# Kernel optimization log

Hardware: AMD Instinct MI355X
Metric: run time of the kernel (lower is better)

The kernel has to match this reference:

```python
import jax, jax.numpy as jnp
import numpy as np

N_NODES = 10000
N_EDGES = 320000
IN_FEATS = 256
NUM_HEADS = 8
OUT_FEATS = 64
NEG_SLOPE = 0.2


def setup_inputs() -> dict:
    key = jax.random.key(0)
    k = jax.random.split(key, 7)
    feat = jax.random.normal(k[0], (N_NODES, IN_FEATS), dtype=jnp.float32)
    W = jax.random.normal(k[1], (IN_FEATS, NUM_HEADS * OUT_FEATS), dtype=jnp.float32) * (1.0 / np.sqrt(IN_FEATS))
    attn_l = jax.random.normal(k[2], (1, NUM_HEADS, OUT_FEATS), dtype=jnp.float32) * 0.1
    attn_r = jax.random.normal(k[3], (1, NUM_HEADS, OUT_FEATS), dtype=jnp.float32) * 0.1
    adj = jax.random.uniform(k[4], (N_NODES, N_NODES), dtype=jnp.float32)
    src = jax.random.randint(k[5], (N_EDGES,), 0, N_NODES, dtype=jnp.int32)
    dst = jax.random.randint(k[6], (N_EDGES,), 0, N_NODES, dtype=jnp.int32)
    return {"feat": feat, "W": W, "attn_l": attn_l, "attn_r": attn_r,
            "adj": adj, "src": src, "dst": dst, "idx": 0}


def reference(feat, W, attn_l, attn_r, adj, src, dst, idx):
    N = feat.shape[0]
    # node projection: [N, H, D]
    ft = (feat @ W).reshape(N, NUM_HEADS, OUT_FEATS)
    # per-node attention logits [N, H]
    el = jnp.sum(ft * attn_l, axis=-1)
    er = jnp.sum(ft * attn_r, axis=-1)
    # u_add_v on edges + LeakyReLU -> [E, H]
    e = el[src] + er[dst]
    e = jnp.where(e > 0, e, NEG_SLOPE * e)
    # edge softmax: segment softmax over destination node
    m = jax.ops.segment_max(e, dst, num_segments=N)          # [N, H]
    ex = jnp.exp(e - m[dst])                                  # [E, H]
    s = jax.ops.segment_sum(ex, dst, num_segments=N)          # [N, H]
    a = ex / s[dst]                                           # [E, H]
    # vectorized adjacency masking (replaces per-edge Python loop)
    a = a * adj[src + idx, dst + idx][:, None]                # [E, H]
    # u_mul_e + scatter-sum aggregation -> [N, H, D]
    msg = ft[src] * a[:, :, None]                             # [E, H, D]
    rst = jax.ops.segment_sum(msg, dst, num_segments=N)
    return rst
```

## Files before the change

kernel.cpp:

```cpp
#include <hip/hip_runtime.h>
#include <hip/hip_bf16.h>
#include <cstdint>
#include <cstddef>

#define IN_FEATS 256
#define NUM_HEADS 8
#define HD 512
#define CH 64
#define ELLCAP 128

typedef __attribute__((ext_vector_type(8))) short bf16x8;
typedef __attribute__((ext_vector_type(4))) float f32x4;

__device__ inline unsigned short bf16_bits(float f) {
    unsigned x = __float_as_uint(f);
    x += 0x7fffu + ((x >> 16) & 1u);
    return (unsigned short)(x >> 16);
}


__global__ __launch_bounds__(256) void k0_kernel(const float* __restrict__ W,
                                                 const float* __restrict__ feat,
                                                 int* __restrict__ deg,
                                                 unsigned short* __restrict__ Wt,
                                                 unsigned short* __restrict__ featb,
                                                 int M) {
    const int b = blockIdx.x;
    const int t = threadIdx.x;
    if (b < 40) {
        int i = b * 256 + t;
        if (i < M) deg[i] = 0;
        return;
    }
    if (b < 72) {
        __shared__ float tile[64][65];
        const int bb = b - 40;
        const int h = bb >> 2;
        const int k0 = (bb & 3) * 64;
#pragma unroll 4
        for (int it = 0; it < 16; ++it) {
            int r = it * 4 + (t >> 6);
            int c = t & 63;
            tile[r][c] = W[(size_t)(k0 + r) * HD + h * 64 + c];
        }
        __syncthreads();
#pragma unroll 4
        for (int it = 0; it < 16; ++it) {
            int c = it * 4 + (t >> 6);
            int k = t & 63;
            Wt[((size_t)h * 64 + c) * IN_FEATS + k0 + k] = bf16_bits(tile[k][c]);
        }
        return;
    }
    {
        size_t base = (size_t)(b - 72) * 1024 + (size_t)t * 4;
        if (base < (size_t)M * IN_FEATS) {
            float4 v = *(const float4*)(feat + base);
            ushort4 o;
            o.x = bf16_bits(v.x);
            o.y = bf16_bits(v.y);
            o.z = bf16_bits(v.z);
            o.w = bf16_bits(v.w);
            *(ushort4*)(featb + base) = o;
        }
    }
}


__global__ __launch_bounds__(256) void k1_kernel(const int* __restrict__ src,
                                                 const int* __restrict__ dst,
                                                 int* __restrict__ deg,
                                                 int* __restrict__ ell,
                                                 const unsigned short* __restrict__ featb,
                                                 const float* __restrict__ al,
                                                 const float* __restrict__ ar,
                                                 const unsigned short* __restrict__ Wt,
                                                 float* __restrict__ el,
                                                 float* __restrict__ er,
                                                 signed char* __restrict__ ftq,
                                                 float* __restrict__ scaleb,
                                                 int E, int M, int nb_ft) {
    const int b = blockIdx.x;
    const int t = threadIdx.x;
    if (b >= nb_ft) {
        int i = (b - nb_ft) * 256 + t;
        if (i < E) {
            int d = dst[i];
            int r = atomicAdd(&deg[d], 1);
            if (r < ELLCAP) ell[(size_t)d * ELLCAP + r] = src[i];
        }
        return;
    }
    {
        const int id = b;
        const int NBX = (M + 63) / 64;
        const int bx = id % NBX;
        const int by = id / NBX;
        const int lane = t & 63, wv = t >> 6;
        const int n0 = bx * 64 + wv * 16;
        const int r = lane & 15;
        const int kg = lane >> 4;
        const int arow = min(n0 + r, M - 1);
        const short* aptr = (const short*)featb + (size_t)arow * IN_FEATS + kg * 8;
        const short* bptr = (const short*)Wt + ((size_t)by * 64 + r) * IN_FEATS + kg * 8;
        f32x4 acc[4];
#pragma unroll
        for (int c = 0; c < 4; ++c) acc[c] = (f32x4){0.f, 0.f, 0.f, 0.f};
#pragma unroll
        for (int kk = 0; kk < 128; kk += 32) {
            bf16x8 a0 = *(const bf16x8*)(aptr + kk);
            bf16x8 a1 = *(const bf16x8*)(aptr + 128 + kk);
#pragma unroll
            for (int c = 0; c < 4; ++c) {
                bf16x8 b0 = *(const bf16x8*)(bptr + (size_t)c * 16 * IN_FEATS + kk);
                bf16x8 b1 = *(const bf16x8*)(bptr + (size_t)c * 16 * IN_FEATS + 128 + kk);
                acc[c] = __builtin_amdgcn_mfma_f32_16x16x32_bf16(a0, b0, acc[c], 0, 0, 0);
                acc[c] = __builtin_amdgcn_mfma_f32_16x16x32_bf16(a1, b1, acc[c], 0, 0, 0);
            }
        }
        float alv[4], arv[4];
#pragma unroll
        for (int c = 0; c < 4; ++c) {
            alv[c] = al[by * 64 + c * 16 + r];
            arv[c] = ar[by * 64 + c * 16 + r];
        }
        float iscale[4], sc[4], pl[4], pr[4];
#pragma unroll
        for (int i = 0; i < 4; ++i) {
            float m = fmaxf(fmaxf(fabsf(acc[0][i]), fabsf(acc[1][i])),
                            fmaxf(fabsf(acc[2][i]), fabsf(acc[3][i])));
            float l = acc[0][i] * alv[0] + acc[1][i] * alv[1] +
                      acc[2][i] * alv[2] + acc[3][i] * alv[3];
            float q = acc[0][i] * arv[0] + acc[1][i] * arv[1] +
                      acc[2][i] * arv[2] + acc[3][i] * arv[3];
#pragma unroll
            for (int off = 1; off < 16; off <<= 1) {
                m = fmaxf(m, __shfl_xor(m, off));
                l += __shfl_xor(l, off);
                q += __shfl_xor(q, off);
            }
            sc[i] = m * (1.0f / 127.0f);
            iscale[i] = (m > 1e-30f) ? (127.0f / m) : 0.f;
            pl[i] = l;
            pr[i] = q;
        }
        const int orow0 = n0 + kg * 4;
        if (r == 0) {
#pragma unroll
            for (int i = 0; i < 4; ++i) {
                int rr = orow0 + i;
                if (rr < M) {
                    scaleb[rr * NUM_HEADS + by] = sc[i];
                    el[rr * NUM_HEADS + by] = pl[i];
                    er[rr * NUM_HEADS + by] = pr[i];
                }
            }
        }
#pragma unroll
        for (int c = 0; c < 4; ++c) {
#pragma unroll
            for (int i = 0; i < 4; ++i) {
                int rr = orow0 + i;
                if (rr < M) {
                    int q = __float2int_rn(acc[c][i] * iscale[i]);
                    q = max(-127, min(127, q));
                    ftq[(size_t)rr * HD + by * 64 + c * 16 + r] = (signed char)q;
                }
            }
        }
    }
}


__global__ __launch_bounds__(256) void agg_kernel(
    const signed char* __restrict__ ftq, const float* __restrict__ scaleb,
    const float* __restrict__ el, const float* __restrict__ er,
    const float* __restrict__ adj, const int* __restrict__ deg,
    const int* __restrict__ ell, const int* __restrict__ idxp,
    float* __restrict__ out, int M) {
    const int n = blockIdx.x;
    const int t = threadIdx.x;
    const int h = t >> 5;
    const int cnt = min(deg[n], ELLCAP);
    if (cnt == 0) {
        *(float2*)(out + (size_t)n * HD + 2 * t) = make_float2(0.f, 0.f);
        return;
    }
    const int lane = t & 63, wv = t >> 6;
    const int j0 = t >> 2;
    const int hg = t & 3;
    const int idx = idxp[0];
    const float* adj_col = adj + (size_t)idx * M + (n + idx);
    const int* erow = ell + (size_t)n * ELLCAP;

    __shared__ float w_lds[2][CH][8];
    __shared__ int s_lds[2][CH];
    __shared__ float partial[4][4][2];
    __shared__ float inv_s[8];

    const float2 er2 = *(const float2*)&er[n * NUM_HEADS + 2 * hg];

    float2 ssum = make_float2(0.f, 0.f);
    float2 acc = make_float2(0.f, 0.f);
    int s_r = 0;
    float2 w_r = make_float2(0.f, 0.f);
    auto stage = [&](int base) {
        int j = base + j0;
        if (j < cnt) {
            s_r = erow[j];
            float2 e2 = *(const float2*)&el[s_r * NUM_HEADS + 2 * hg];
            float2 sc2 = *(const float2*)&scaleb[s_r * NUM_HEADS + 2 * hg];
            float av = adj_col[(size_t)s_r * M];
            float ex = e2.x + er2.x; ex = (ex > 0.f) ? ex : 0.2f * ex;
            float ey = e2.y + er2.y; ey = (ey > 0.f) ? ey : 0.2f * ey;
            float px = __expf(ex), py = __expf(ey);
            ssum.x += px; ssum.y += py;
            w_r = make_float2(px * av * sc2.x, py * av * sc2.y);
        }
    };
    auto write_lds = [&](int buf, int base) {
        int j = base + j0;
        if (j < cnt) {
            *(float2*)&w_lds[buf][j0][2 * hg] = w_r;
            if (hg == 0) s_lds[buf][j0] = s_r;
        }
    };
    int buf = 0;
    stage(0);
    write_lds(0, 0);
    __syncthreads();
    for (int base = 0; base < cnt; base += CH) {
        const bool more = (base + CH) < cnt;
        if (more) stage(base + CH);
        int c = min(CH, cnt - base);
        const int* srow = &s_lds[buf][0];
        const float* wrow = &w_lds[buf][0][0];
#pragma unroll 4
        for (int jj = 0; jj < c; ++jj) {
            int s = srow[jj];
            unsigned short v = *(const unsigned short*)(ftq + (size_t)s * HD + 2 * t);
            float fx = (float)(signed char)(v & 0xff);
            float fy = (float)(signed char)(v >> 8);
            float w = wrow[jj * 8 + h];
            acc.x = fmaf(w, fx, acc.x);
            acc.y = fmaf(w, fy, acc.y);
        }
        if (more) {
            write_lds(buf ^ 1, base + CH);
            __syncthreads();
            buf ^= 1;
        }
    }
    float sx = ssum.x, sy = ssum.y;
#pragma unroll
    for (int off = 4; off < 64; off <<= 1) {
        sx += __shfl_xor(sx, off);
        sy += __shfl_xor(sy, off);
    }
    if (lane < 4) {
        partial[wv][hg][0] = sx;
        partial[wv][hg][1] = sy;
    }
    __syncthreads();
    if (t < 8) {
        int hgg = t >> 1, comp = t & 1;
        inv_s[t] = 1.f / (partial[0][hgg][comp] + partial[1][hgg][comp] +
                          partial[2][hgg][comp] + partial[3][hgg][comp]);
    }
    __syncthreads();
    const float inv = inv_s[h];
    *(float2*)(out + (size_t)n * HD + 2 * t) = make_float2(acc.x * inv, acc.y * inv);
}


extern "C" void kernel_launch(void* const* d_in, const int* in_sizes, int n_in,
                              void* d_out, int out_size, void* d_ws, size_t ws_size,
                              hipStream_t stream) {
    const float* feat   = (const float*)d_in[0];
    const float* W      = (const float*)d_in[1];
    const float* attn_l = (const float*)d_in[2];
    const float* attn_r = (const float*)d_in[3];
    const float* adj    = (const float*)d_in[4];
    const int*   src    = (const int*)d_in[5];
    const int*   dst    = (const int*)d_in[6];
    const int*   idxp   = (const int*)d_in[7];
    float* out = (float*)d_out;

    const int M = in_sizes[0] / IN_FEATS;
    const int E = in_sizes[5];

    char* ws = (char*)d_ws;
    size_t off = 0;
    auto alloc = [&](size_t bytes) -> void* {
        off = (off + 255) & ~(size_t)255;
        void* p = ws + off;
        off += bytes;
        return p;
    };
    signed char* ftq      = (signed char*)alloc((size_t)M * HD);
    unsigned short* featb = (unsigned short*)alloc((size_t)M * IN_FEATS * sizeof(short));
    float* scaleb         = (float*)alloc((size_t)M * NUM_HEADS * sizeof(float));
    unsigned short* Wt    = (unsigned short*)alloc((size_t)HD * IN_FEATS * sizeof(short));
    float* el        = (float*)alloc((size_t)M * NUM_HEADS * sizeof(float));
    float* er        = (float*)alloc((size_t)M * NUM_HEADS * sizeof(float));
    int*   deg       = (int*)alloc((size_t)M * sizeof(int));
    int*   ell       = (int*)alloc((size_t)M * ELLCAP * sizeof(int));

    const int nb_cv = ((int)((size_t)M * IN_FEATS / 1024));
    k0_kernel<<<72 + nb_cv, 256, 0, stream>>>(W, feat, deg, Wt, featb, M);

    const int nb_sc = (E + 255) / 256;
    const int NBX = (M + 63) / 64;
    const int nb_ft = NBX * NUM_HEADS;
    k1_kernel<<<nb_ft + nb_sc, 256, 0, stream>>>(src, dst, deg, ell,
                                                 featb, attn_l, attn_r, Wt, el, er,
                                                 ftq, scaleb, E, M, nb_ft);

    agg_kernel<<<M, 256, 0, stream>>>(ftq, scaleb, el, er, adj, deg, ell, idxp, out, M);
}
```

Baseline: 89.79 us.

## Fuse feat bf16 conversion into GEMM and compute four heads per block

The separate fp32-to-bf16 conversion pass over feat and its workspace buffer are removed. The projection kernel now loads fp32 feat directly, converts it to bf16 in registers, and keeps the A fragments resident while each block computes four heads instead of one. This cuts a full write and read of the bf16 copy, and it reads feat twice rather than eight times. In exchange, GEMM blocks drop to a quarter as many and each uses far more accumulator registers (64 floats plus 8 A fragments), which may lower occupancy.

```diff
diff --git a/kernel.cpp b/kernel.cpp
--- a/kernel.cpp
+++ b/kernel.cpp
@@ -20,10 +20,8 @@
 
 
 __global__ __launch_bounds__(256) void k0_kernel(const float* __restrict__ W,
-                                                 const float* __restrict__ feat,
                                                  int* __restrict__ deg,
                                                  unsigned short* __restrict__ Wt,
-                                                 unsigned short* __restrict__ featb,
                                                  int M) {
     const int b = blockIdx.x;
     const int t = threadIdx.x;
@@ -32,37 +30,22 @@
         if (i < M) deg[i] = 0;
         return;
     }
-    if (b < 72) {
-        __shared__ float tile[64][65];
-        const int bb = b - 40;
-        const int h = bb >> 2;
-        const int k0 = (bb & 3) * 64;
+    __shared__ float tile[64][65];
+    const int bb = b - 40;
+    const int h = bb >> 2;
+    const int k0 = (bb & 3) * 64;
 #pragma unroll 4
-        for (int it = 0; it < 16; ++it) {
-            int r = it * 4 + (t >> 6);
-            int c = t & 63;
-            tile[r][c] = W[(size_t)(k0 + r) * HD + h * 64 + c];
-        }
-        __syncthreads();
+    for (int it = 0; it < 16; ++it) {
+        int r = it * 4 + (t >> 6);
+        int c = t & 63;
+        tile[r][c] = W[(size_t)(k0 + r) * HD + h * 64 + c];
+    }
+    __syncthreads();
 #pragma unroll 4
-        for (int it = 0; it < 16; ++it) {
-            int c = it * 4 + (t >> 6);
-            int k = t & 63;
-            Wt[((size_t)h * 64 + c) * IN_FEATS + k0 + k] = bf16_bits(tile[k][c]);
-        }
-        return;
-    }
-    {
-        size_t base = (size_t)(b - 72) * 1024 + (size_t)t * 4;
-        if (base < (size_t)M * IN_FEATS) {
-            float4 v = *(const float4*)(feat + base);
-            ushort4 o;
-            o.x = bf16_bits(v.x);
-            o.y = bf16_bits(v.y);
-            o.z = bf16_bits(v.z);
-            o.w = bf16_bits(v.w);
-            *(ushort4*)(featb + base) = o;
-        }
+    for (int it = 0; it < 16; ++it) {
+        int c = it * 4 + (t >> 6);
+        int k = t & 63;
+        Wt[((size_t)h * 64 + c) * IN_FEATS + k0 + k] = bf16_bits(tile[k][c]);
     }
 }
 
@@ -71,7 +54,7 @@
                                                  const int* __restrict__ dst,
                                                  int* __restrict__ deg,
                                                  int* __restrict__ ell,
-                                                 const unsigned short* __restrict__ featb,
+                                                 const float* __restrict__ feat,
                                                  const float* __restrict__ al,
                                                  const float* __restrict__ ar,
                                                  const unsigned short* __restrict__ Wt,
@@ -92,79 +75,98 @@
         return;
     }
     {
-        const int id = b;
         const int NBX = (M + 63) / 64;
-        const int bx = id % NBX;
-        const int by = id / NBX;
+        const int bx = b % NBX;
+        const int hg2 = b / NBX;
         const int lane = t & 63, wv = t >> 6;
         const int n0 = bx * 64 + wv * 16;
         const int r = lane & 15;
         const int kg = lane >> 4;
         const int arow = min(n0 + r, M - 1);
-        const short* aptr = (const short*)featb + (size_t)arow * IN_FEATS + kg * 8;
-        const short* bptr = (const short*)Wt + ((size_t)by * 64 + r) * IN_FEATS + kg * 8;
-        f32x4 acc[4];
-#pragma unroll
-        for (int c = 0; c < 4; ++c) acc[c] = (f32x4){0.f, 0.f, 0.f, 0.f};
-#pragma unroll
-        for (int kk = 0; kk < 128; kk += 32) {
-            bf16x8 a0 = *(const bf16x8*)(aptr + kk);
-            bf16x8 a1 = *(const bf16x8*)(aptr + 128 + kk);
+        const float* aptr = feat + (size_t)arow * IN_FEATS + kg * 8;
+
+        bf16x8 afrag[8];
+#pragma unroll
+        for (int ks = 0; ks < 8; ++ks) {
+            float4 a0 = *(const float4*)(aptr + ks * 32);
+            float4 a1 = *(const float4*)(aptr + ks * 32 + 4);
+            unsigned short* ap = (unsigned short*)&afrag[ks];
+            ap[0] = bf16_bits(a0.x); ap[1] = bf16_bits(a0.y);
+            ap[2] = bf16_bits(a0.z); ap[3] = bf16_bits(a0.w);
+            ap[4] = bf16_bits(a1.x); ap[5] = bf16_bits(a1.y);
+            ap[6] = bf16_bits(a1.z); ap[7] = bf16_bits(a1.w);
+        }
+
+        f32x4 acc[4][4];
+#pragma unroll
+        for (int hh = 0; hh < 4; ++hh)
+#pragma unroll
+            for (int c = 0; c < 4; ++c) acc[hh][c] = (f32x4){0.f, 0.f, 0.f, 0.f};
+
+        const short* bbase = (const short*)Wt + ((size_t)(hg2 * 4) * 64 + r) * IN_FEATS + kg * 8;
+#pragma unroll
+        for (int ks = 0; ks < 8; ++ks) {
+#pragma unroll
+            for (int hh = 0; hh < 4; ++hh) {
+#pragma unroll
+                for (int c = 0; c < 4; ++c) {
+                    bf16x8 bb = *(const bf16x8*)(bbase + ((size_t)hh * 64 + (size_t)c * 16) * IN_FEATS + ks * 32);
+                    acc[hh][c] = __builtin_amdgcn_mfma_f32_16x16x32_bf16(afrag[ks], bb, acc[hh][c], 0, 0, 0);
+                }
+            }
+        }
+
+        const int orow0 = n0 + kg * 4;
+#pragma unroll
+        for (int hh = 0; hh < 4; ++hh) {
+            const int by = hg2 * 4 + hh;
+            float alv[4], arv[4];
 #pragma unroll
             for (int c = 0; c < 4; ++c) {
-                bf16x8 b0 = *(const bf16x8*)(bptr + (size_t)c * 16 * IN_FEATS + kk);
-                bf16x8 b1 = *(const bf16x8*)(bptr + (size_t)c * 16 * IN_FEATS + 128 + kk);
-                acc[c] = __builtin_amdgcn_mfma_f32_16x16x32_bf16(a0, b0, acc[c], 0, 0, 0);
-                acc[c] = __builtin_amdgcn_mfma_f32_16x16x32_bf16(a1, b1, acc[c], 0, 0, 0);
-            }
-        }
-        float alv[4], arv[4];
-#pragma unroll
-        for (int c = 0; c < 4; ++c) {
-            alv[c] = al[by * 64 + c * 16 + r];
-            arv[c] = ar[by * 64 + c * 16 + r];
-        }
-        float iscale[4], sc[4], pl[4], pr[4];
-#pragma unroll
-        for (int i = 0; i < 4; ++i) {
-            float m = fmaxf(fmaxf(fabsf(acc[0][i]), fabsf(acc[1][i])),
-                            fmaxf(fabsf(acc[2][i]), fabsf(acc[3][i])));
-            float l = acc[0][i] * alv[0] + acc[1][i] * alv[1] +
-                      acc[2][i] * alv[2] + acc[3][i] * alv[3];
-            float q = acc[0][i] * arv[0] + acc[1][i] * arv[1] +
-                      acc[2][i] * arv[2] + acc[3][i] * arv[3];
-#pragma unroll
-            for (int off = 1; off < 16; off <<= 1) {
-                m = fmaxf(m, __shfl_xor(m, off));
-                l += __shfl_xor(l, off);
-                q += __shfl_xor(q, off);
-            }
-            sc[i] = m * (1.0f / 127.0f);
-            iscale[i] = (m > 1e-30f) ? (127.0f / m) : 0.f;
-            pl[i] = l;
-            pr[i] = q;
-        }
-        const int orow0 = n0 + kg * 4;
-        if (r == 0) {
+                alv[c] = al[by * 64 + c * 16 + r];
+                arv[c] = ar[by * 64 + c * 16 + r];
+            }
+            float iscale[4], sc[4], pl[4], pr[4];
 #pragma unroll
             for (int i = 0; i < 4; ++i) {
-                int rr = orow0 + i;
-                if (rr < M) {
-                    scaleb[rr * NUM_HEADS + by] = sc[i];
-                    el[rr * NUM_HEADS + by] = pl[i];
-                    er[rr * NUM_HEADS + by] = pr[i];
+                float m = fmaxf(fmaxf(fabsf(acc[hh][0][i]), fabsf(acc[hh][1][i])),
+                                fmaxf(fabsf(acc[hh][2][i]), fabsf(acc[hh][3][i])));
+                float l = acc[hh][0][i] * alv[0] + acc[hh][1][i] * alv[1] +
+                          acc[hh][2][i] * alv[2] + acc[hh][3][i] * alv[3];
+                float q = acc[hh][0][i] * arv[0] + acc[hh][1][i] * arv[1] +
+                          acc[hh][2][i] * arv[2] + acc[hh][3][i] * arv[3];
+#pragma unroll
+                for (int off = 1; off < 16; off <<= 1) {
+                    m = fmaxf(m, __shfl_xor(m, off));
+                    l += __shfl_xor(l, off);
+                    q += __shfl_xor(q, off);
                 }
-            }
-        }
-#pragma unroll
-        for (int c = 0; c < 4; ++c) {
-#pragma unroll
-            for (int i = 0; i < 4; ++i) {
-                int rr = orow0 + i;
-                if (rr < M) {
-                    int q = __float2int_rn(acc[c][i] * iscale[i]);
-                    q = max(-127, min(127, q));
-                    ftq[(size_t)rr * HD + by * 64 + c * 16 + r] = (signed char)q;
+                sc[i] = m * (1.0f / 127.0f);
+                iscale[i] = (m > 1e-30f) ? (127.0f / m) : 0.f;
+                pl[i] = l;
+                pr[i] = q;
+            }
+            if (r == 0) {
+#pragma unroll
+                for (int i = 0; i < 4; ++i) {
+                    int rr = orow0 + i;
+                    if (rr < M) {
+                        scaleb[rr * NUM_HEADS + by] = sc[i];
+                        el[rr * NUM_HEADS + by] = pl[i];
+                        er[rr * NUM_HEADS + by] = pr[i];
+                    }
+                }
+            }
+#pragma unroll
+            for (int c = 0; c < 4; ++c) {
+#pragma unroll
+                for (int i = 0; i < 4; ++i) {
+                    int rr = orow0 + i;
+                    if (rr < M) {
+                        int q = __float2int_rn(acc[hh][c][i] * iscale[i]);
+                        q = max(-127, min(127, q));
+                        ftq[(size_t)rr * HD + by * 64 + c * 16 + r] = (signed char)q;
+                    }
                 }
             }
         }
@@ -297,23 +299,21 @@
         off += bytes;
         return p;
     };
-    signed char* ftq      = (signed char*)alloc((size_t)M * HD);
-    unsigned short* featb = (unsigned short*)alloc((size_t)M * IN_FEATS * sizeof(short));
-    float* scaleb         = (float*)alloc((size_t)M * NUM_HEADS * sizeof(float));
-    unsigned short* Wt    = (unsigned short*)alloc((size_t)HD * IN_FEATS * sizeof(short));
+    signed char* ftq    = (signed char*)alloc((size_t)M * HD);
+    float* scaleb       = (float*)alloc((size_t)M * NUM_HEADS * sizeof(float));
+    unsigned short* Wt  = (unsigned short*)alloc((size_t)HD * IN_FEATS * sizeof(short));
     float* el        = (float*)alloc((size_t)M * NUM_HEADS * sizeof(float));
     float* er        = (float*)alloc((size_t)M * NUM_HEADS * sizeof(float));
     int*   deg       = (int*)alloc((size_t)M * sizeof(int));
     int*   ell       = (int*)alloc((size_t)M * ELLCAP * sizeof(int));
 
-    const int nb_cv = ((int)((size_t)M * IN_FEATS / 1024));
-    k0_kernel<<<72 + nb_cv, 256, 0, stream>>>(W, feat, deg, Wt, featb, M);
+    k0_kernel<<<72, 256, 0, stream>>>(W, deg, Wt, M);
 
     const int nb_sc = (E + 255) / 256;
     const int NBX = (M + 63) / 64;
-    const int nb_ft = NBX * NUM_HEADS;
+    const int nb_ft = NBX * 2;
     k1_kernel<<<nb_ft + nb_sc, 256, 0, stream>>>(src, dst, deg, ell,
-                                                 featb, attn_l, attn_r, Wt, el, er,
+                                                 feat, attn_l, attn_r, Wt, el, er,
                                                  ftq, scaleb, E, M, nb_ft);
 
     agg_kernel<<<M, 256, 0, stream>>>(ftq, scaleb, el, er, adj, deg, ell, idxp, out, M);
```

Result: no change. 91.10 us (+1.5%).

## Fuse feat bf16 conversion into GEMM, split ELL into 16-bit segmented buckets

Applied to the files above, without the earlier changes.

Removes the separate fp32-to-bf16 pass over feat and converts feat to bf16 inside the MFMA projection loop. It also splits each node's degree counter into four sub-counters, chosen by edge index, to spread atomic contention, and stores neighbor indices as 16-bit values in four 32-slot segments. The aggregation kernel rebuilds the neighbor order from the four segment counts. The trade-offs are extra conversion ALU work and more feat reads across the eight head blocks, a per-segment cap of 32 that could drop edges on high-degree nodes, and 16-bit indices that only work while M is at most 65536.

```diff
diff --git a/kernel.cpp b/kernel.cpp
--- a/kernel.cpp
+++ b/kernel.cpp
@@ -7,7 +7,8 @@
 #define NUM_HEADS 8
 #define HD 512
 #define CH 64
-#define ELLCAP 128
+#define SEGCAP 32
+#define ROWCAP 128
 
 typedef __attribute__((ext_vector_type(8))) short bf16x8;
 typedef __attribute__((ext_vector_type(4))) float f32x4;
@@ -20,58 +21,42 @@
 
 
 __global__ __launch_bounds__(256) void k0_kernel(const float* __restrict__ W,
-                                                 const float* __restrict__ feat,
-                                                 int* __restrict__ deg,
+                                                 int* __restrict__ deg4,
                                                  unsigned short* __restrict__ Wt,
-                                                 unsigned short* __restrict__ featb,
                                                  int M) {
     const int b = blockIdx.x;
     const int t = threadIdx.x;
-    if (b < 40) {
+    const int nz = M * 4;
+    if (b < 157) {
         int i = b * 256 + t;
-        if (i < M) deg[i] = 0;
+        if (i < nz) deg4[i] = 0;
         return;
     }
-    if (b < 72) {
-        __shared__ float tile[64][65];
-        const int bb = b - 40;
-        const int h = bb >> 2;
-        const int k0 = (bb & 3) * 64;
+    __shared__ float tile[64][65];
+    const int bb = b - 157;
+    const int h = bb >> 2;
+    const int k0 = (bb & 3) * 64;
 #pragma unroll 4
-        for (int it = 0; it < 16; ++it) {
-            int r = it * 4 + (t >> 6);
-            int c = t & 63;
-            tile[r][c] = W[(size_t)(k0 + r) * HD + h * 64 + c];
-        }
-        __syncthreads();
+    for (int it = 0; it < 16; ++it) {
+        int r = it * 4 + (t >> 6);
+        int c = t & 63;
+        tile[r][c] = W[(size_t)(k0 + r) * HD + h * 64 + c];
+    }
+    __syncthreads();
 #pragma unroll 4
-        for (int it = 0; it < 16; ++it) {
-            int c = it * 4 + (t >> 6);
-            int k = t & 63;
-            Wt[((size_t)h * 64 + c) * IN_FEATS + k0 + k] = bf16_bits(tile[k][c]);
-        }
-        return;
-    }
-    {
-        size_t base = (size_t)(b - 72) * 1024 + (size_t)t * 4;
-        if (base < (size_t)M * IN_FEATS) {
-            float4 v = *(const float4*)(feat + base);
-            ushort4 o;
-            o.x = bf16_bits(v.x);
-            o.y = bf16_bits(v.y);
-            o.z = bf16_bits(v.z);
-            o.w = bf16_bits(v.w);
-            *(ushort4*)(featb + base) = o;
-        }
+    for (int it = 0; it < 16; ++it) {
+        int c = it * 4 + (t >> 6);
+        int k = t & 63;
+        Wt[((size_t)h * 64 + c) * IN_FEATS + k0 + k] = bf16_bits(tile[k][c]);
     }
 }
 
 
 __global__ __launch_bounds__(256) void k1_kernel(const int* __restrict__ src,
                                                  const int* __restrict__ dst,
-                                                 int* __restrict__ deg,
-                                                 int* __restrict__ ell,
-                                                 const unsigned short* __restrict__ featb,
+                                                 int* __restrict__ deg4,
+                                                 unsigned short* __restrict__ ell16,
+                                                 const float* __restrict__ feat,
                                                  const float* __restrict__ al,
                                                  const float* __restrict__ ar,
                                                  const unsigned short* __restrict__ Wt,
@@ -86,8 +71,10 @@
         int i = (b - nb_ft) * 256 + t;
         if (i < E) {
             int d = dst[i];
-            int r = atomicAdd(&deg[d], 1);
-            if (r < ELLCAP) ell[(size_t)d * ELLCAP + r] = src[i];
+            int g = i & 3;
+            int r = atomicAdd(&deg4[d * 4 + g], 1);
+            if (r < SEGCAP)
+                ell16[(size_t)d * ROWCAP + g * SEGCAP + r] = (unsigned short)src[i];
         }
         return;
     }
@@ -101,21 +88,25 @@
         const int r = lane & 15;
         const int kg = lane >> 4;
         const int arow = min(n0 + r, M - 1);
-        const short* aptr = (const short*)featb + (size_t)arow * IN_FEATS + kg * 8;
+        const float* aptr = feat + (size_t)arow * IN_FEATS + kg * 8;
         const short* bptr = (const short*)Wt + ((size_t)by * 64 + r) * IN_FEATS + kg * 8;
         f32x4 acc[4];
 #pragma unroll
         for (int c = 0; c < 4; ++c) acc[c] = (f32x4){0.f, 0.f, 0.f, 0.f};
 #pragma unroll
-        for (int kk = 0; kk < 128; kk += 32) {
-            bf16x8 a0 = *(const bf16x8*)(aptr + kk);
-            bf16x8 a1 = *(const bf16x8*)(aptr + 128 + kk);
+        for (int kk = 0; kk < IN_FEATS; kk += 32) {
+            float4 a0 = *(const float4*)(aptr + kk);
+            float4 a1 = *(const float4*)(aptr + kk + 4);
+            bf16x8 a;
+            unsigned short* ap = (unsigned short*)&a;
+            ap[0] = bf16_bits(a0.x); ap[1] = bf16_bits(a0.y);
+            ap[2] = bf16_bits(a0.z); ap[3] = bf16_bits(a0.w);
+            ap[4] = bf16_bits(a1.x); ap[5] = bf16_bits(a1.y);
+            ap[6] = bf16_bits(a1.z); ap[7] = bf16_bits(a1.w);
 #pragma unroll
             for (int c = 0; c < 4; ++c) {
-                bf16x8 b0 = *(const bf16x8*)(bptr + (size_t)c * 16 * IN_FEATS + kk);
-                bf16x8 b1 = *(const bf16x8*)(bptr + (size_t)c * 16 * IN_FEATS + 128 + kk);
-                acc[c] = __builtin_amdgcn_mfma_f32_16x16x32_bf16(a0, b0, acc[c], 0, 0, 0);
-                acc[c] = __builtin_amdgcn_mfma_f32_16x16x32_bf16(a1, b1, acc[c], 0, 0, 0);
+                bf16x8 bb = *(const bf16x8*)(bptr + (size_t)c * 16 * IN_FEATS + kk);
+                acc[c] = __builtin_amdgcn_mfma_f32_16x16x32_bf16(a, bb, acc[c], 0, 0, 0);
             }
         }
         float alv[4], arv[4];
@@ -175,13 +166,17 @@
 __global__ __launch_bounds__(256) void agg_kernel(
     const signed char* __restrict__ ftq, const float* __restrict__ scaleb,
     const float* __restrict__ el, const float* __restrict__ er,
-    const float* __restrict__ adj, const int* __restrict__ deg,
-    const int* __restrict__ ell, const int* __restrict__ idxp,
+    const float* __restrict__ adj, const int* __restrict__ deg4,
+    const unsigned short* __restrict__ ell16, const int* __restrict__ idxp,
     float* __restrict__ out, int M) {
     const int n = blockIdx.x;
     const int t = threadIdx.x;
     const int h = t >> 5;
-    const int cnt = min(deg[n], ELLCAP);
+    const int4 c4 = *(const int4*)&deg4[n * 4];
+    const int c0 = min(c4.x, SEGCAP), c1 = min(c4.y, SEGCAP);
+    const int c2 = min(c4.z, SEGCAP), c3 = min(c4.w, SEGCAP);
+    const int p0 = c0, p1 = c0 + c1, p2 = c0 + c1 + c2;
+    const int cnt = p2 + c3;
     if (cnt == 0) {
         *(float2*)(out + (size_t)n * HD + 2 * t) = make_float2(0.f, 0.f);
         return;
@@ -191,7 +186,7 @@
     const int hg = t & 3;
     const int idx = idxp[0];
     const float* adj_col = adj + (size_t)idx * M + (n + idx);
-    const int* erow = ell + (size_t)n * ELLCAP;
+    const unsigned short* erow = ell16 + (size_t)n * ROWCAP;
 
     __shared__ float w_lds[2][CH][8];
     __shared__ int s_lds[2][CH];
@@ -207,7 +202,12 @@
     auto stage = [&](int base) {
         int j = base + j0;
         if (j < cnt) {
-            s_r = erow[j];
+            int seg, off;
+            if (j < p0) { seg = 0; off = j; }
+            else if (j < p1) { seg = 1; off = j - p0; }
+            else if (j < p2) { seg = 2; off = j - p1; }
+            else { seg = 3; off = j - p2; }
+            s_r = erow[seg * SEGCAP + off];
             float2 e2 = *(const float2*)&el[s_r * NUM_HEADS + 2 * hg];
             float2 sc2 = *(const float2*)&scaleb[s_r * NUM_HEADS + 2 * hg];
             float av = adj_col[(size_t)s_r * M];
@@ -298,23 +298,21 @@
         return p;
     };
     signed char* ftq      = (signed char*)alloc((size_t)M * HD);
-    unsigned short* featb = (unsigned short*)alloc((size_t)M * IN_FEATS * sizeof(short));
     float* scaleb         = (float*)alloc((size_t)M * NUM_HEADS * sizeof(float));
     unsigned short* Wt    = (unsigned short*)alloc((size_t)HD * IN_FEATS * sizeof(short));
+    unsigned short* ell16 = (unsigned short*)alloc((size_t)M * ROWCAP * sizeof(short));
     float* el        = (float*)alloc((size_t)M * NUM_HEADS * sizeof(float));
     float* er        = (float*)alloc((size_t)M * NUM_HEADS * sizeof(float));
-    int*   deg       = (int*)alloc((size_t)M * sizeof(int));
-    int*   ell       = (int*)alloc((size_t)M * ELLCAP * sizeof(int));
-
-    const int nb_cv = ((int)((size_t)M * IN_FEATS / 1024));
-    k0_kernel<<<72 + nb_cv, 256, 0, stream>>>(W, feat, deg, Wt, featb, M);
+    int*   deg4      = (int*)alloc((size_t)M * 4 * sizeof(int));
+
+    k0_kernel<<<189, 256, 0, stream>>>(W, deg4, Wt, M);
 
     const int nb_sc = (E + 255) / 256;
     const int NBX = (M + 63) / 64;
     const int nb_ft = NBX * NUM_HEADS;
-    k1_kernel<<<nb_ft + nb_sc, 256, 0, stream>>>(src, dst, deg, ell,
-                                                 featb, attn_l, attn_r, Wt, el, er,
+    k1_kernel<<<nb_ft + nb_sc, 256, 0, stream>>>(src, dst, deg4, ell16,
+                                                 feat, attn_l, attn_r, Wt, el, er,
                                                  ftq, scaleb, E, M, nb_ft);
 
-    agg_kernel<<<M, 256, 0, stream>>>(ftq, scaleb, el, er, adj, deg, ell, idxp, out, M);
-}
+    agg_kernel<<<M, 256, 0, stream>>>(ftq, scaleb, el, er, adj, deg4, ell16, idxp, out, M);
+}
```

After: 88.27 us. No clear change (-1.7%).
